# Kernel optimization log

Hardware: AMD Instinct MI355X
Metric: run time of the kernel (lower is better)

## Reference

```python
import jax, jax.numpy as jnp
import numpy as np

B, N, C, H = 4, 2048, 768, 12
D = C // H  # head_dim = 64

def setup_inputs() -> dict:
    key = jax.random.key(0)
    ks = jax.random.split(key, 6)
    s = 0.02
    return {
        "img_tokens": jax.random.normal(ks[0], (B, N, C), jnp.float32),
        "ln_gamma": jnp.ones((C,), jnp.float32),
        "ln_beta": jnp.zeros((C,), jnp.float32),
        "w_qkv": jax.random.normal(ks[1], (C, 3 * C), jnp.float32) * s,
        "w_out": jax.random.normal(ks[2], (C, C), jnp.float32) * s,
        "b_out": jnp.zeros((C,), jnp.float32),
    }

def reference(img_tokens, ln_gamma, ln_beta, w_qkv, w_out, b_out):
    x = img_tokens
    # LayerNorm over channel dim
    mu = jnp.mean(x, axis=-1, keepdims=True)
    var = jnp.var(x, axis=-1, keepdims=True)
    xn = (x - mu) * jax.lax.rsqrt(var + 1e-5) * ln_gamma + ln_beta
    qkv = xn @ w_qkv                      # [B, N, 3C]
    q, k, v = jnp.split(qkv, 3, axis=-1)
    def heads(t):                          # [B, N, C] -> [B, H, N, D]
        return t.reshape(B, N, H, D).transpose(0, 2, 1, 3)
    q, k, v = heads(q), heads(k), heads(v)
    scale = 1.0 / np.sqrt(D).astype(np.float32)
    scores = jnp.einsum('bhnd,bhmd->bhnm', q, k) * scale  # [B, H, N, N]
    attn = jax.nn.softmax(scores, axis=-1)
    out = jnp.einsum('bhnm,bhmd->bhnd', attn, v)          # [B, H, N, D]
    out = out.transpose(0, 2, 1, 3).reshape(B, N, C)
    out = out @ w_out + b_out
    return out + img_tokens
```

## Files before the change

kernel.cpp:

```cpp
#include <hip/hip_runtime.h>


typedef __bf16 bf16x8 __attribute__((ext_vector_type(8)));
typedef float  f32x4  __attribute__((ext_vector_type(4)));

#define MFMA16(a,b,c) __builtin_amdgcn_mfma_f32_16x16x32_bf16((a),(b),(c),0,0,0)

__device__ inline f32x4 zero4() { f32x4 z = {0.f,0.f,0.f,0.f}; return z; }

__device__ inline void gll16(const __bf16* g, __bf16* l) {
  __builtin_amdgcn_global_load_lds((const __attribute__((address_space(1))) unsigned int*)g,
                                   (__attribute__((address_space(3))) unsigned int*)l,
                                   16, 0, 0);
}

__device__ inline __bf16 bf16_trunc(float f) {
  const unsigned int u = __builtin_bit_cast(unsigned int, f);
  return __builtin_bit_cast(__bf16, (unsigned short)(u >> 16));
}

__global__ __launch_bounds__(256) void ln_kernel(const float* __restrict__ x,
                                                 const float* __restrict__ g,
                                                 const float* __restrict__ bt,
                                                 __bf16* __restrict__ xn) {
  const int row = blockIdx.x;
  const int tid = threadIdx.x;
  const float* xr = x + (size_t)row * 768;
  float v[3]; float s = 0.f, ss = 0.f;
  #pragma unroll
  for (int i = 0; i < 3; ++i) { float f = xr[tid + 256*i]; v[i] = f; s += f; ss += f*f; }
  #pragma unroll
  for (int m = 32; m >= 1; m >>= 1) { s += __shfl_xor(s, m, 64); ss += __shfl_xor(ss, m, 64); }
  __shared__ float red[8];
  const int wave = tid >> 6;
  if ((tid & 63) == 0) { red[wave] = s; red[4 + wave] = ss; }
  __syncthreads();
  s  = red[0] + red[1] + red[2] + red[3];
  ss = red[4] + red[5] + red[6] + red[7];
  const float mu  = s * (1.f/768.f);
  const float var = ss * (1.f/768.f) - mu*mu;
  const float inv = rsqrtf(var + 1e-5f);
  __bf16* xo = xn + (size_t)row * 768;
  #pragma unroll
  for (int i = 0; i < 3; ++i) {
    const int c0 = tid + 256*i;
    xo[c0] = (__bf16)((v[i] - mu) * inv * g[c0] + bt[c0]);
  }
}

__global__ __launch_bounds__(256) void transpose_kernel(const float* __restrict__ in,
                                                        __bf16* __restrict__ out,
                                                        int R, int C) {
  __shared__ float t[32][33];
  const int tx = threadIdx.x & 31, ty = threadIdx.x >> 5;
  const int c0 = blockIdx.x * 32, r0 = blockIdx.y * 32;
  #pragma unroll
  for (int p = 0; p < 4; ++p) t[ty + 8*p][tx] = in[(size_t)(r0 + ty + 8*p) * C + c0 + tx];
  __syncthreads();
  #pragma unroll
  for (int p = 0; p < 4; ++p) out[(size_t)(c0 + ty + 8*p) * R + r0 + tx] = (__bf16)t[tx][ty + 8*p];
}

template<int KDIM>
__device__ inline void gemm_mainloop(const __bf16* __restrict__ A, const __bf16* __restrict__ BT,
                                     int bm, int bn, int wave, int lane,
                                     f32x4 acc[4][4], __bf16* Asm, __bf16* Bsm) {
  const int wm = wave >> 1, wn = wave & 1;
  const int lr = lane & 15, lk = lane >> 4;
  for (int k0 = 0; k0 < KDIM; k0 += 64) {
    #pragma unroll
    for (int s2 = 0; s2 < 4; ++s2) {
      const int st = wave * 4 + s2;
      const int rb = st >> 1, kh = st & 1;
      gll16(A  + (size_t)(bm + rb*16 + lr) * KDIM + k0 + kh*32 + lk*8, Asm + st*512);
      gll16(BT + (size_t)(bn + rb*16 + lr) * KDIM + k0 + kh*32 + lk*8, Bsm + st*512);
    }
    __builtin_amdgcn_s_waitcnt(0);
    __syncthreads();
    #pragma unroll
    for (int ks = 0; ks < 2; ++ks) {
      bf16x8 a[4], b[4];
      #pragma unroll
      for (int mt = 0; mt < 4; ++mt) a[mt] = *(const bf16x8*)(Asm + ((wm*4+mt)*2+ks)*512 + lane*8);
      #pragma unroll
      for (int nt = 0; nt < 4; ++nt) b[nt] = *(const bf16x8*)(Bsm + ((wn*4+nt)*2+ks)*512 + lane*8);
      #pragma unroll
      for (int mt = 0; mt < 4; ++mt)
        #pragma unroll
        for (int nt = 0; nt < 4; ++nt)
          acc[mt][nt] = MFMA16(a[mt], b[nt], acc[mt][nt]);
    }
    __syncthreads();
  }
}

__global__ __launch_bounds__(256) void gemm_qkv_kernel(const __bf16* __restrict__ A,
                                                       const __bf16* __restrict__ BT,
                                                       __bf16* __restrict__ q,
                                                       __bf16* __restrict__ k,
                                                       __bf16* __restrict__ vt) {
  __shared__ __align__(16) __bf16 smem[2*8192];
  __bf16* Asm = smem;
  __bf16* Bsm = smem + 8192;
  const int lane = threadIdx.x & 63, wave = threadIdx.x >> 6;
  const int bm = blockIdx.y * 128, bn = blockIdx.x * 128;
  f32x4 acc[4][4];
  #pragma unroll
  for (int i = 0; i < 4; ++i)
    #pragma unroll
    for (int j = 0; j < 4; ++j) acc[i][j] = zero4();
  gemm_mainloop<768>(A, BT, bm, bn, wave, lane, acc, Asm, Bsm);
  const int wm = wave >> 1, wn = wave & 1;
  const int quad = lane >> 4, c = lane & 15;
  if (bn < 1536) {
    const float qscale = 0.125f * 1.44269504088896f;
    #pragma unroll
    for (int mt = 0; mt < 4; ++mt)
      #pragma unroll
      for (int nt = 0; nt < 4; ++nt) {
        const int col = bn + wn*64 + nt*16 + c;
        const int which = col >= 768 ? 1 : 0;
        const int within = col - which*768;
        const int h = within >> 6, d = within & 63;
        #pragma unroll
        for (int r = 0; r < 4; ++r) {
          const int row = bm + wm*64 + mt*16 + quad*4 + r;
          const int b = row >> 11, n = row & 2047;
          const float vv = acc[mt][nt][r];
          const size_t idx = ((size_t)(b*12 + h) * 2048 + n) * 64 + d;
          if (which == 0) q[idx] = (__bf16)(vv * qscale);
          else            k[idx] = (__bf16)vv;
        }
      }
  } else {
    __syncthreads();
    #pragma unroll
    for (int mt = 0; mt < 4; ++mt)
      #pragma unroll
      for (int nt = 0; nt < 4; ++nt) {
        const int lcol = wn*64 + nt*16 + c;
        #pragma unroll
        for (int r = 0; r < 4; ++r) {
          const int lrow = wm*64 + mt*16 + quad*4 + r;
          smem[lrow*66 + lcol] = (__bf16)acc[mt][nt][r];
        }
      }
    __syncthreads();
    const int b = bm >> 11, n0 = bm & 2047;
    const int vo = bn - 1536;
    const int n = threadIdx.x & 127;
    const int csel = threadIdx.x >> 7;
    #pragma unroll
    for (int pass = 0; pass < 64; ++pass) {
      const int lc = pass*2 + csel;
      const int gcol = vo + lc;
      const int h = gcol >> 6, d = gcol & 63;
      vt[((size_t)(b*12 + h)*64 + d)*2048 + n0 + n] = smem[n*66 + lc];
    }
  }
}

__global__ __launch_bounds__(256) void gemm_out_kernel(const __bf16* __restrict__ A,
                                                       const __bf16* __restrict__ BT,
                                                       const float* __restrict__ bias,
                                                       const float* __restrict__ resid,
                                                       float* __restrict__ out) {
  __shared__ __align__(16) __bf16 Asm[16*512];
  __shared__ __align__(16) __bf16 Bsm[16*512];
  const int lane = threadIdx.x & 63, wave = threadIdx.x >> 6;
  const int bm = blockIdx.y * 128, bn = blockIdx.x * 128;
  f32x4 acc[4][4];
  #pragma unroll
  for (int i = 0; i < 4; ++i)
    #pragma unroll
    for (int j = 0; j < 4; ++j) acc[i][j] = zero4();
  gemm_mainloop<768>(A, BT, bm, bn, wave, lane, acc, Asm, Bsm);
  const int wm = wave >> 1, wn = wave & 1;
  const int quad = lane >> 4, c = lane & 15;
  #pragma unroll
  for (int mt = 0; mt < 4; ++mt)
    #pragma unroll
    for (int nt = 0; nt < 4; ++nt) {
      const int col = bn + wn*64 + nt*16 + c;
      #pragma unroll
      for (int r = 0; r < 4; ++r) {
        const int row = bm + wm*64 + mt*16 + quad*4 + r;
        out[(size_t)row*768 + col] = acc[mt][nt][r] + bias[col] + resid[(size_t)row*768 + col];
      }
    }
}

__global__ __launch_bounds__(256) void attn_kernel(const __bf16* __restrict__ q,
                                                   const __bf16* __restrict__ k,
                                                   const __bf16* __restrict__ vt,
                                                   __bf16* __restrict__ o) {
  const int xcd = blockIdx.x & 7, i = blockIdx.x >> 3;
  const int bh = xcd * 6 + (i >> 4);
  const int qt = i & 15;
  const int lane = threadIdx.x & 63, wave = threadIdx.x >> 6;
  const int c = lane & 15, quad = lane >> 4;
  const int lr = lane & 15, lk = lane >> 4;
  const int q0 = qt*128 + wave*32;

  const __bf16* qb = q  + ((size_t)bh*2048 + q0) * 64;
  const __bf16* kb = k  + (size_t)bh * 2048 * 64;
  const __bf16* vb = vt + (size_t)bh * 64 * 2048;

  __shared__ __align__(16) __bf16 Ksm[2][4096];
  __shared__ __align__(16) __bf16 Vsm[2][4096];
  __shared__ __align__(16) __bf16 plds[4][1024];
  __bf16* myp = plds[wave];

  bf16x8 aq[2][2];
  #pragma unroll
  for (int rg = 0; rg < 2; ++rg) {
    aq[rg][0] = *(const bf16x8*)(qb + (size_t)(rg*16 + c)*64 + quad*8);
    aq[rg][1] = *(const bf16x8*)(qb + (size_t)(rg*16 + c)*64 + 32 + quad*8);
  }

  float cl[2][4];
  f32x4 od[2][4];
  #pragma unroll
  for (int rg = 0; rg < 2; ++rg)
    #pragma unroll
    for (int r = 0; r < 4; ++r) { cl[rg][r] = 0.f; od[rg][r] = zero4(); }

  auto stage = [&](int it) {
    const int kt = it * 64;
    __bf16* Ks = Ksm[it & 1];
    __bf16* Vs = Vsm[it & 1];
    gll16(kb + (size_t)(kt + wave*16 + lr) * 64 + lk*8,        Ks + (wave*2+0)*512);
    gll16(kb + (size_t)(kt + wave*16 + lr) * 64 + 32 + lk*8,   Ks + (wave*2+1)*512);
    gll16(vb + (size_t)(wave*16 + lr) * 2048 + kt + lk*8,      Vs + (wave*2+0)*512);
    gll16(vb + (size_t)(wave*16 + lr) * 2048 + kt + 32 + lk*8, Vs + (wave*2+1)*512);
  };

  stage(0);
  stage(1);

  const int sl = lane ^ ((lane >> 3) & 7);

  for (int it = 0; it < 32; ++it) {
    const __bf16* Ks = Ksm[it & 1];
    const __bf16* Vs = Vsm[it & 1];
    if (it < 31) asm volatile("s_waitcnt vmcnt(4)" ::: "memory");
    else         asm volatile("s_waitcnt vmcnt(0)" ::: "memory");
    asm volatile("s_barrier" ::: "memory");
    #pragma unroll
    for (int ch = 0; ch < 2; ++ch) {
      f32x4 s0[2], s1[2];
      #pragma unroll
      for (int t2 = 0; t2 < 2; ++t2) {
        const int t = ch*2 + t2;
        const bf16x8 b0 = *(const bf16x8*)(Ks + (t*2+0)*512 + lane*8);
        const bf16x8 b1 = *(const bf16x8*)(Ks + (t*2+1)*512 + lane*8);
        f32x4 z0 = zero4(), z1 = zero4();
        z0 = MFMA16(aq[0][0], b0, z0); z0 = MFMA16(aq[0][1], b1, z0);
        z1 = MFMA16(aq[1][0], b0, z1); z1 = MFMA16(aq[1][1], b1, z1);
        s0[t2] = z0; s1[t2] = z1;
      }
      #pragma unroll
      for (int t2 = 0; t2 < 2; ++t2) {
        const int kk = t2*16 + c;
        const int k8 = kk >> 3, j = kk & 7;
        #pragma unroll
        for (int r = 0; r < 4; ++r) {
          const int row = quad*4 + r;
          const int b = k8*16 + row;
          const int sb = b ^ ((b >> 3) & 7);
          const float p0 = __builtin_amdgcn_exp2f(s0[t2][r]);
          const float p1 = __builtin_amdgcn_exp2f(s1[t2][r]);
          cl[0][r] += p0; cl[1][r] += p1;
          myp[sb*8 + j]       = bf16_trunc(p0);
          myp[512 + sb*8 + j] = bf16_trunc(p1);
        }
      }
      asm volatile("s_waitcnt lgkmcnt(0)" ::: "memory");
      const bf16x8 ap0 = *(const bf16x8*)(myp + sl*8);
      const bf16x8 ap1 = *(const bf16x8*)(myp + 512 + sl*8);
      asm volatile("" ::: "memory");
      #pragma unroll
      for (int dt = 0; dt < 4; ++dt) {
        const bf16x8 bv = *(const bf16x8*)(Vs + (dt*2+ch)*512 + lane*8);
        od[0][dt] = MFMA16(ap0, bv, od[0][dt]);
        od[1][dt] = MFMA16(ap1, bv, od[1][dt]);
      }
    }
    asm volatile("s_barrier" ::: "memory");
    if (it + 2 < 32) stage(it + 2);
  }
  const int b = bh / 12, h = bh % 12;
  #pragma unroll
  for (int rg = 0; rg < 2; ++rg) {
    float rl[4];
    #pragma unroll
    for (int r = 0; r < 4; ++r) {
      float v0 = cl[rg][r];
      v0 += __shfl_xor(v0, 1); v0 += __shfl_xor(v0, 2);
      v0 += __shfl_xor(v0, 4); v0 += __shfl_xor(v0, 8);
      rl[r] = 1.f / v0;
    }
    #pragma unroll
    for (int dt = 0; dt < 4; ++dt)
      #pragma unroll
      for (int r = 0; r < 4; ++r) {
        const int n = q0 + rg*16 + quad*4 + r;
        const int col = h*64 + dt*16 + c;
        o[((size_t)b*2048 + n)*768 + col] = (__bf16)(od[rg][dt][r] * rl[r]);
      }
  }
}

extern "C" void kernel_launch(void* const* d_in, const int* in_sizes, int n_in,
                              void* d_out, int out_size, void* d_ws, size_t ws_size,
                              hipStream_t stream) {
  const float* img   = (const float*)d_in[0];
  const float* gamma = (const float*)d_in[1];
  const float* beta  = (const float*)d_in[2];
  const float* wqkv  = (const float*)d_in[3];
  const float* wout  = (const float*)d_in[4];
  const float* bout  = (const float*)d_in[5];
  float* out = (float*)d_out;

  __bf16* ws = (__bf16*)d_ws;
  size_t off = 0;
  __bf16* xn    = ws + off; off += (size_t)8192*768;
  __bf16* wqkvT = ws + off; off += (size_t)2304*768;
  __bf16* woutT = ws + off; off += (size_t)768*768;
  __bf16* qs    = ws + off; off += (size_t)48*2048*64;
  __bf16* ks    = ws + off; off += (size_t)48*2048*64;
  __bf16* vts   = ws + off; off += (size_t)48*64*2048;
  __bf16* os    = ws + off; off += (size_t)8192*768;

  ln_kernel<<<8192, 256, 0, stream>>>(img, gamma, beta, xn);
  transpose_kernel<<<dim3(72, 24), 256, 0, stream>>>(wqkv, wqkvT, 768, 2304);
  transpose_kernel<<<dim3(24, 24), 256, 0, stream>>>(wout, woutT, 768, 768);
  gemm_qkv_kernel<<<dim3(18, 64), 256, 0, stream>>>(xn, wqkvT, qs, ks, vts);
  attn_kernel<<<768, 256, 0, stream>>>(qs, ks, vts, os);
  gemm_out_kernel<<<dim3(6, 64), 256, 0, stream>>>(os, woutT, bout, img, out);
}
```

Before: 269.4 us.

## Split attention over key halves with a combine kernel, and fuse the prep kernels

The attention kernel now splits each (batch, head, query-tile) job into two halves over the key range, doubling the grid. It writes unnormalized partial outputs in bf16 plus row sums, and a new combine kernel adds the halves and normalizes. This is valid because the softmax uses no running max. The LayerNorm and both weight-transpose kernels are merged into one launch that picks its role by block index. Dead workspace buffers are reused for the partials. The change trades extra global traffic, an extra launch and an extra bf16 rounding of the partials for more parallel blocks in attention and fewer launches.

```diff
diff --git a/kernel.cpp b/kernel.cpp
--- a/kernel.cpp
+++ b/kernel.cpp
@@ -19,46 +19,56 @@
   return __builtin_bit_cast(__bf16, (unsigned short)(u >> 16));
 }
 
-__global__ __launch_bounds__(256) void ln_kernel(const float* __restrict__ x,
-                                                 const float* __restrict__ g,
-                                                 const float* __restrict__ bt,
-                                                 __bf16* __restrict__ xn) {
-  const int row = blockIdx.x;
+__global__ __launch_bounds__(256) void prep_kernel(const float* __restrict__ x,
+                                                   const float* __restrict__ g,
+                                                   const float* __restrict__ bt,
+                                                   const float* __restrict__ wqkv,
+                                                   const float* __restrict__ wout,
+                                                   __bf16* __restrict__ xn,
+                                                   __bf16* __restrict__ wqkvT,
+                                                   __bf16* __restrict__ woutT) {
+  __shared__ float t[32][33];
   const int tid = threadIdx.x;
-  const float* xr = x + (size_t)row * 768;
-  float v[3]; float s = 0.f, ss = 0.f;
-  #pragma unroll
-  for (int i = 0; i < 3; ++i) { float f = xr[tid + 256*i]; v[i] = f; s += f; ss += f*f; }
-  #pragma unroll
-  for (int m = 32; m >= 1; m >>= 1) { s += __shfl_xor(s, m, 64); ss += __shfl_xor(ss, m, 64); }
-  __shared__ float red[8];
-  const int wave = tid >> 6;
-  if ((tid & 63) == 0) { red[wave] = s; red[4 + wave] = ss; }
-  __syncthreads();
-  s  = red[0] + red[1] + red[2] + red[3];
-  ss = red[4] + red[5] + red[6] + red[7];
-  const float mu  = s * (1.f/768.f);
-  const float var = ss * (1.f/768.f) - mu*mu;
-  const float inv = rsqrtf(var + 1e-5f);
-  __bf16* xo = xn + (size_t)row * 768;
-  #pragma unroll
-  for (int i = 0; i < 3; ++i) {
-    const int c0 = tid + 256*i;
-    xo[c0] = (__bf16)((v[i] - mu) * inv * g[c0] + bt[c0]);
-  }
-}
-
-__global__ __launch_bounds__(256) void transpose_kernel(const float* __restrict__ in,
-                                                        __bf16* __restrict__ out,
-                                                        int R, int C) {
-  __shared__ float t[32][33];
-  const int tx = threadIdx.x & 31, ty = threadIdx.x >> 5;
-  const int c0 = blockIdx.x * 32, r0 = blockIdx.y * 32;
-  #pragma unroll
-  for (int p = 0; p < 4; ++p) t[ty + 8*p][tx] = in[(size_t)(r0 + ty + 8*p) * C + c0 + tx];
-  __syncthreads();
-  #pragma unroll
-  for (int p = 0; p < 4; ++p) out[(size_t)(c0 + ty + 8*p) * R + r0 + tx] = (__bf16)t[tx][ty + 8*p];
+  if (blockIdx.x < 8192) {
+    const int row = blockIdx.x;
+    const float* xr = x + (size_t)row * 768;
+    float v[3]; float s = 0.f, ss = 0.f;
+    #pragma unroll
+    for (int i = 0; i < 3; ++i) { float f = xr[tid + 256*i]; v[i] = f; s += f; ss += f*f; }
+    #pragma unroll
+    for (int m = 32; m >= 1; m >>= 1) { s += __shfl_xor(s, m, 64); ss += __shfl_xor(ss, m, 64); }
+    float* red = &t[0][0];
+    const int wave = tid >> 6;
+    if ((tid & 63) == 0) { red[wave] = s; red[4 + wave] = ss; }
+    __syncthreads();
+    s  = red[0] + red[1] + red[2] + red[3];
+    ss = red[4] + red[5] + red[6] + red[7];
+    const float mu  = s * (1.f/768.f);
+    const float var = ss * (1.f/768.f) - mu*mu;
+    const float inv = rsqrtf(var + 1e-5f);
+    __bf16* xo = xn + (size_t)row * 768;
+    #pragma unroll
+    for (int i = 0; i < 3; ++i) {
+      const int c0 = tid + 256*i;
+      xo[c0] = (__bf16)((v[i] - mu) * inv * g[c0] + bt[c0]);
+    }
+  } else {
+    const float* in; __bf16* out; int R, C, cx, ry;
+    if (blockIdx.x < 8192 + 1728) {
+      const int i = blockIdx.x - 8192;
+      in = wqkv; out = wqkvT; R = 768; C = 2304; cx = i % 72; ry = i / 72;
+    } else {
+      const int i = blockIdx.x - 8192 - 1728;
+      in = wout; out = woutT; R = 768; C = 768; cx = i % 24; ry = i / 24;
+    }
+    const int tx = tid & 31, ty = tid >> 5;
+    const int c0 = cx * 32, r0 = ry * 32;
+    #pragma unroll
+    for (int p = 0; p < 4; ++p) t[ty + 8*p][tx] = in[(size_t)(r0 + ty + 8*p) * C + c0 + tx];
+    __syncthreads();
+    #pragma unroll
+    for (int p = 0; p < 4; ++p) out[(size_t)(c0 + ty + 8*p) * R + r0 + tx] = (__bf16)t[tx][ty + 8*p];
+  }
 }
 
 template<int KDIM>
@@ -193,14 +203,18 @@
 __global__ __launch_bounds__(256) void attn_kernel(const __bf16* __restrict__ q,
                                                    const __bf16* __restrict__ k,
                                                    const __bf16* __restrict__ vt,
-                                                   __bf16* __restrict__ o) {
+                                                   __bf16* __restrict__ odp0,
+                                                   __bf16* __restrict__ odp1,
+                                                   float* __restrict__ clp) {
   const int xcd = blockIdx.x & 7, i = blockIdx.x >> 3;
-  const int bh = xcd * 6 + (i >> 4);
+  const int grp = xcd * 12 + (i >> 4);
   const int qt = i & 15;
+  const int bh = grp >> 1, half = grp & 1;
   const int lane = threadIdx.x & 63, wave = threadIdx.x >> 6;
   const int c = lane & 15, quad = lane >> 4;
   const int lr = lane & 15, lk = lane >> 4;
   const int q0 = qt*128 + wave*32;
+  const int kbase = half * 1024;
 
   const __bf16* qb = q  + ((size_t)bh*2048 + q0) * 64;
   const __bf16* kb = k  + (size_t)bh * 2048 * 64;
@@ -226,7 +240,7 @@
     for (int r = 0; r < 4; ++r) { cl[rg][r] = 0.f; od[rg][r] = zero4(); }
 
   auto stage = [&](int it) {
-    const int kt = it * 64;
+    const int kt = kbase + it * 64;
     __bf16* Ks = Ksm[it & 1];
     __bf16* Vs = Vsm[it & 1];
     gll16(kb + (size_t)(kt + wave*16 + lr) * 64 + lk*8,        Ks + (wave*2+0)*512);
@@ -240,10 +254,10 @@
 
   const int sl = lane ^ ((lane >> 3) & 7);
 
-  for (int it = 0; it < 32; ++it) {
+  for (int it = 0; it < 16; ++it) {
     const __bf16* Ks = Ksm[it & 1];
     const __bf16* Vs = Vsm[it & 1];
-    if (it < 31) asm volatile("s_waitcnt vmcnt(4)" ::: "memory");
+    if (it < 15) asm volatile("s_waitcnt vmcnt(4)" ::: "memory");
     else         asm volatile("s_waitcnt vmcnt(0)" ::: "memory");
     asm volatile("s_barrier" ::: "memory");
     #pragma unroll
@@ -287,28 +301,44 @@
       }
     }
     asm volatile("s_barrier" ::: "memory");
-    if (it + 2 < 32) stage(it + 2);
-  }
-  const int b = bh / 12, h = bh % 12;
+    if (it + 2 < 16) stage(it + 2);
+  }
+  __bf16* odp = half ? odp1 : odp0;
+  float* clh = clp + (size_t)(half*48 + bh) * 2048;
   #pragma unroll
   for (int rg = 0; rg < 2; ++rg) {
-    float rl[4];
+    float lv[4];
     #pragma unroll
     for (int r = 0; r < 4; ++r) {
       float v0 = cl[rg][r];
       v0 += __shfl_xor(v0, 1); v0 += __shfl_xor(v0, 2);
       v0 += __shfl_xor(v0, 4); v0 += __shfl_xor(v0, 8);
-      rl[r] = 1.f / v0;
-    }
-    #pragma unroll
-    for (int dt = 0; dt < 4; ++dt)
-      #pragma unroll
-      for (int r = 0; r < 4; ++r) {
-        const int n = q0 + rg*16 + quad*4 + r;
-        const int col = h*64 + dt*16 + c;
-        o[((size_t)b*2048 + n)*768 + col] = (__bf16)(od[rg][dt][r] * rl[r]);
-      }
-  }
+      lv[r] = v0;
+    }
+    #pragma unroll
+    for (int r = 0; r < 4; ++r) {
+      const int n = q0 + rg*16 + quad*4 + r;
+      if (c == 0) clh[n] = lv[r];
+      #pragma unroll
+      for (int dt = 0; dt < 4; ++dt)
+        odp[((size_t)bh*2048 + n)*64 + dt*16 + c] = (__bf16)od[rg][dt][r];
+    }
+  }
+}
+
+__global__ __launch_bounds__(256) void combine_kernel(const __bf16* __restrict__ odp0,
+                                                      const __bf16* __restrict__ odp1,
+                                                      const float* __restrict__ clp,
+                                                      __bf16* __restrict__ o) {
+  const int rnum = blockIdx.x * 4 + (threadIdx.x >> 6);
+  const int d = threadIdx.x & 63;
+  const int bh = rnum >> 11, n = rnum & 2047;
+  const int b = bh / 12, h = bh % 12;
+  const size_t ridx = (size_t)rnum * 64 + d;
+  const float l0 = clp[(size_t)bh*2048 + n];
+  const float l1 = clp[(size_t)(48 + bh)*2048 + n];
+  const float v = ((float)odp0[ridx] + (float)odp1[ridx]) * __frcp_rn(l0 + l1);
+  o[((size_t)b*2048 + n)*768 + h*64 + d] = (__bf16)v;
 }
 
 extern "C" void kernel_launch(void* const* d_in, const int* in_sizes, int n_in,
@@ -332,10 +362,14 @@
   __bf16* vts   = ws + off; off += (size_t)48*64*2048;
   __bf16* os    = ws + off; off += (size_t)8192*768;
 
-  ln_kernel<<<8192, 256, 0, stream>>>(img, gamma, beta, xn);
-  transpose_kernel<<<dim3(72, 24), 256, 0, stream>>>(wqkv, wqkvT, 768, 2304);
-  transpose_kernel<<<dim3(24, 24), 256, 0, stream>>>(wout, woutT, 768, 768);
+  __bf16* odp0 = os;
+  __bf16* odp1 = xn;
+  float*  clp  = (float*)wqkvT;
+  __bf16* attn_out = ks;
+
+  prep_kernel<<<10496, 256, 0, stream>>>(img, gamma, beta, wqkv, wout, xn, wqkvT, woutT);
   gemm_qkv_kernel<<<dim3(18, 64), 256, 0, stream>>>(xn, wqkvT, qs, ks, vts);
-  attn_kernel<<<768, 256, 0, stream>>>(qs, ks, vts, os);
-  gemm_out_kernel<<<dim3(6, 64), 256, 0, stream>>>(os, woutT, bout, img, out);
-}
+  attn_kernel<<<1536, 256, 0, stream>>>(qs, ks, vts, odp0, odp1, clp);
+  combine_kernel<<<24576, 256, 0, stream>>>(odp0, odp1, clp, attn_out);
+  gemm_out_kernel<<<dim3(6, 64), 256, 0, stream>>>(attn_out, woutT, bout, img, out);
+}
```

After: 278.1 us. +3.2%, slower.
